# Optimization experiments

Measured on AMD Instinct MI355X. Metric: run time of the kernel, lower is better.

Reference implementation:

```python
import jax, jax.numpy as jnp
import numpy as np

B = 131072          # batch
T = 1024            # num_task_types
D = 1029            # input_dim = 5 + T  (4 scalar feats + contention effect + T one-hot)
H1, H2 = 64, 32     # hidden_dims


def setup_inputs() -> dict:
    key = jax.random.key(0)
    ks = jax.random.split(key, 8)
    x = jax.random.normal(ks[0], (B, D), dtype=jnp.float32)
    contention = jax.random.normal(ks[1], (T, T), dtype=jnp.float32) * 0.1
    # MLP params (Linear uses y = x @ W.T + b in torch; we store W as (in, out))
    w1 = jax.random.normal(ks[2], (D, H1), dtype=jnp.float32) * (1.0 / np.sqrt(D))
    b1 = jnp.zeros((H1,), dtype=jnp.float32)
    w2 = jax.random.normal(ks[3], (H1, H2), dtype=jnp.float32) * (1.0 / np.sqrt(H1))
    b2 = jnp.zeros((H2,), dtype=jnp.float32)
    w3 = jax.random.normal(ks[4], (H2, 1), dtype=jnp.float32) * (1.0 / np.sqrt(H2))
    b3 = jnp.zeros((1,), dtype=jnp.float32)
    return {"x": x, "contention": contention,
            "w1": w1, "b1": b1, "w2": w2, "b2": b2, "w3": w3, "b3": b3}


def reference(x, contention, w1, b1, w2, b2, w3, b3):
    feats = x[:, :4]                          # density, recent_latency, diversity, time_since_same
    density = x[:, 0:1]                       # (B, 1)
    task_onehot = x[:, 4:4 + T]               # (B, T)
    task_id = jnp.argmax(task_onehot, axis=1) # (B,) int
    # vectorized replacement of the per-sample python loop:
    # gather row, mean over columns, scale by density
    contention_effect = jnp.mean(contention[task_id], axis=1, keepdims=True) * density  # (B, 1)
    combined = jnp.concatenate([feats, contention_effect, task_onehot], axis=1)  # (B, 5+T) == (B, D)
    # MLP (dropout is identity in eval mode)
    h = jax.nn.relu(combined @ w1 + b1)
    h = jax.nn.relu(h @ w2 + b2)
    latency = jax.nn.relu(h @ w3 + b3)        # (B, 1)
    return latency[:, 0]                      # squeeze -> (B,)
```

## Files before the change

kernel.cpp:

```cpp
#include <hip/hip_runtime.h>

typedef __bf16 bf16x8 __attribute__((ext_vector_type(8)));
typedef float f32x4 __attribute__((ext_vector_type(4)));

#define ROW_F 1029
#define TMB 64
#define NKB 33

__global__ __launch_bounds__(256) void k_rowmean(const float* __restrict__ cont,
                                                 float* __restrict__ rowmean) {
    __shared__ float red[4];
    int row = blockIdx.x;
    const float4* cr = (const float4*)(cont + (size_t)row * 1024);
    float4 v = cr[threadIdx.x];
    float p = v.x + v.y + v.z + v.w;
    for (int m = 1; m < 64; m <<= 1) p += __shfl_xor(p, m, 64);
    int lane = threadIdx.x & 63, wid = threadIdx.x >> 6;
    if (lane == 0) red[wid] = p;
    __syncthreads();
    if (threadIdx.x == 0)
        rowmean[row] = (red[0] + red[1] + red[2] + red[3]) * (1.0f / 1024.0f);
}

__global__ __launch_bounds__(256) void k_wpack(const float* __restrict__ w1,
                                               __bf16* __restrict__ wfrag) {
    int o = blockIdx.x * 256 + threadIdx.x;
    int j    = o & 7;
    int lane = (o >> 3) & 63;
    int nt   = (o >> 9) & 3;
    int kb   = o >> 11;
    int k = kb * 32 + ((lane >> 4) << 3) + j;
    int n = nt * 16 + (lane & 15);
    float val = 0.0f;
    if (k < 4)          val = w1[k * 64 + n];
    else if (k < 1028)  val = w1[(k + 1) * 64 + n];
    wfrag[o] = (__bf16)val;
}

__global__ __launch_bounds__(256, 4) void k_main(const float* __restrict__ x,
                                                 const float* __restrict__ w1,
                                                 const float* __restrict__ b1,
                                                 const float* __restrict__ w2,
                                                 const float* __restrict__ b2,
                                                 const float* __restrict__ w3,
                                                 const float* __restrict__ b3,
                                                 const float* __restrict__ rowmean,
                                                 const __bf16* __restrict__ wfrag,
                                                 float* __restrict__ out) {
    __shared__ float h1_lds[TMB * 65];

    const int tid = threadIdx.x;
    const int l   = tid & 63;
    const int w   = tid >> 6;
    const int m0  = l & 15;
    const int c   = l >> 4;

    const int row = blockIdx.x * TMB + w * 16 + m0;
    const float* xr = x + (size_t)row * ROW_F + c * 8;
    const f32x4* wfp = (const f32x4*)wfrag;

    f32x4 acc0 = {0.f,0.f,0.f,0.f}, acc1 = {0.f,0.f,0.f,0.f};
    f32x4 acc2 = {0.f,0.f,0.f,0.f}, acc3 = {0.f,0.f,0.f,0.f};
    float best = -1e30f; int bidx = 4; float dens = 0.f;

    {
        float v[8];
        #pragma unroll
        for (int j = 0; j < 8; ++j) v[j] = xr[j];
        if (c == 0) dens = v[0];
        bf16x8 af;
        #pragma unroll
        for (int j = 0; j < 8; ++j) {
            af[j] = (__bf16)v[j];
            int k = c * 8 + j;
            bool ok = (k >= 4) && (v[j] > best);
            best = ok ? v[j] : best;
            bidx = ok ? k : bidx;
        }
        acc0 = __builtin_amdgcn_mfma_f32_16x16x32_bf16(af, __builtin_bit_cast(bf16x8, wfp[0*64 + l]), acc0, 0,0,0);
        acc1 = __builtin_amdgcn_mfma_f32_16x16x32_bf16(af, __builtin_bit_cast(bf16x8, wfp[1*64 + l]), acc1, 0,0,0);
        acc2 = __builtin_amdgcn_mfma_f32_16x16x32_bf16(af, __builtin_bit_cast(bf16x8, wfp[2*64 + l]), acc2, 0,0,0);
        acc3 = __builtin_amdgcn_mfma_f32_16x16x32_bf16(af, __builtin_bit_cast(bf16x8, wfp[3*64 + l]), acc3, 0,0,0);
    }

    for (int kb = 1; kb < 32; ++kb) {
        const float* p = xr + kb * 32;
        float v[8];
        #pragma unroll
        for (int j = 0; j < 8; ++j) v[j] = p[j];
        bf16x8 af;
        int kbase = kb * 32 + c * 8;
        #pragma unroll
        for (int j = 0; j < 8; ++j) {
            af[j] = (__bf16)v[j];
            bool gt = v[j] > best;
            best = gt ? v[j] : best;
            bidx = gt ? (kbase + j) : bidx;
        }
        acc0 = __builtin_amdgcn_mfma_f32_16x16x32_bf16(af, __builtin_bit_cast(bf16x8, wfp[(kb*4+0)*64 + l]), acc0, 0,0,0);
        acc1 = __builtin_amdgcn_mfma_f32_16x16x32_bf16(af, __builtin_bit_cast(bf16x8, wfp[(kb*4+1)*64 + l]), acc1, 0,0,0);
        acc2 = __builtin_amdgcn_mfma_f32_16x16x32_bf16(af, __builtin_bit_cast(bf16x8, wfp[(kb*4+2)*64 + l]), acc2, 0,0,0);
        acc3 = __builtin_amdgcn_mfma_f32_16x16x32_bf16(af, __builtin_bit_cast(bf16x8, wfp[(kb*4+3)*64 + l]), acc3, 0,0,0);
    }

    {
        bf16x8 af;
        #pragma unroll
        for (int j = 0; j < 8; ++j) af[j] = (__bf16)0.f;
        if (c == 0) {
            const float* p = xr + 32 * 32;
            #pragma unroll
            for (int j = 0; j < 4; ++j) {
                float v = p[j];
                af[j] = (__bf16)v;
                bool gt = v > best;
                best = gt ? v : best;
                bidx = gt ? (1024 + j) : bidx;
            }
        }
        acc0 = __builtin_amdgcn_mfma_f32_16x16x32_bf16(af, __builtin_bit_cast(bf16x8, wfp[(32*4+0)*64 + l]), acc0, 0,0,0);
        acc1 = __builtin_amdgcn_mfma_f32_16x16x32_bf16(af, __builtin_bit_cast(bf16x8, wfp[(32*4+1)*64 + l]), acc1, 0,0,0);
        acc2 = __builtin_amdgcn_mfma_f32_16x16x32_bf16(af, __builtin_bit_cast(bf16x8, wfp[(32*4+2)*64 + l]), acc2, 0,0,0);
        acc3 = __builtin_amdgcn_mfma_f32_16x16x32_bf16(af, __builtin_bit_cast(bf16x8, wfp[(32*4+3)*64 + l]), acc3, 0,0,0);
    }

    #pragma unroll
    for (int off = 16; off < 64; off <<= 1) {
        float ob = __shfl_xor(best, off, 64);
        int   oi = __shfl_xor(bidx, off, 64);
        if (ob > best || (ob == best && oi < bidx)) { best = ob; bidx = oi; }
    }
    float ce = 0.f;
    if (c == 0) ce = rowmean[bidx - 4] * dens;

    float ce_r[4];
    #pragma unroll
    for (int r = 0; r < 4; ++r) ce_r[r] = __shfl(ce, c * 4 + r, 64);

    {
        const f32x4* accs[4] = {&acc0, &acc1, &acc2, &acc3};
        #pragma unroll
        for (int nt = 0; nt < 4; ++nt) {
            int n = nt * 16 + m0;
            float w14 = w1[4 * 64 + n];
            float bb  = b1[n];
            #pragma unroll
            for (int r = 0; r < 4; ++r) {
                int m = c * 4 + r;
                float hv = (*accs[nt])[r] + ce_r[r] * w14 + bb;
                h1_lds[(w * 16 + m) * 65 + n] = fmaxf(hv, 0.0f);
            }
        }
    }
    __syncthreads();

    {
        int s  = tid & 15;
        int n2 = s * 2;
        #pragma unroll
        for (int it = 0; it < 4; ++it) {
            int r2 = it * 16 + (tid >> 4);
            float a0 = b2[n2], a1 = b2[n2 + 1];
            const float* hrow = &h1_lds[r2 * 65];
            #pragma unroll 8
            for (int k = 0; k < 64; ++k) {
                float hv = hrow[k];
                float2 wv = *(const float2*)(w2 + k * 32 + n2);
                a0 = fmaf(hv, wv.x, a0);
                a1 = fmaf(hv, wv.y, a1);
            }
            a0 = fmaxf(a0, 0.f); a1 = fmaxf(a1, 0.f);
            float p = a0 * w3[n2] + a1 * w3[n2 + 1];
            p += __shfl_xor(p, 1, 64);
            p += __shfl_xor(p, 2, 64);
            p += __shfl_xor(p, 4, 64);
            p += __shfl_xor(p, 8, 64);
            if (s == 0) out[blockIdx.x * TMB + r2] = fmaxf(p + b3[0], 0.f);
        }
    }
}

extern "C" void kernel_launch(void* const* d_in, const int* in_sizes, int n_in,
                              void* d_out, int out_size, void* d_ws, size_t ws_size,
                              hipStream_t stream) {
    const float* x    = (const float*)d_in[0];
    const float* cont = (const float*)d_in[1];
    const float* w1   = (const float*)d_in[2];
    const float* b1   = (const float*)d_in[3];
    const float* w2   = (const float*)d_in[4];
    const float* b2   = (const float*)d_in[5];
    const float* w3   = (const float*)d_in[6];
    const float* b3   = (const float*)d_in[7];

    __bf16* wfrag   = (__bf16*)d_ws;
    float*  rowmean = (float*)((char*)d_ws + 135168);

    int B = in_sizes[0] / ROW_F;
    float* out = (float*)d_out;

    hipLaunchKernelGGL(k_rowmean, dim3(1024),    dim3(256), 0, stream, cont, rowmean);
    hipLaunchKernelGGL(k_wpack,   dim3(264),     dim3(256), 0, stream, w1, wfrag);
    hipLaunchKernelGGL(k_main,    dim3(B / TMB), dim3(256), 0, stream,
                       x, w1, b1, w2, b2, w3, b3, rowmean, wfrag, out);
}
```

Before: 782.0 us.

## Coalesce x loads via per-wave LDS slab with register prefetch

Each wave now loads its 16 rows of x in coalesced 32-float row segments, using nontemporal loads with a one-block register prefetch. It then transposes them through a per-wave LDS slab into the MFMA A-fragment layout. This replaces the earlier scattered 8-float per-lane strided reads. The layer-2 stage uses per-wave LDS with no block-wide barrier, and launch_bounds drops the occupancy hint. The cost is extra LDS traffic and possibly more register pressure.

After: 792.2 us. About the same (+1.3%).

```diff
diff --git a/kernel.cpp b/kernel.cpp
--- a/kernel.cpp
+++ b/kernel.cpp
@@ -4,8 +4,7 @@
 typedef float f32x4 __attribute__((ext_vector_type(4)));
 
 #define ROW_F 1029
-#define TMB 64
-#define NKB 33
+#define SLAB_STRIDE 36
 
 __global__ __launch_bounds__(256) void k_rowmean(const float* __restrict__ cont,
                                                  float* __restrict__ rowmean) {
@@ -37,91 +36,105 @@
     wfrag[o] = (__bf16)val;
 }
 
-__global__ __launch_bounds__(256, 4) void k_main(const float* __restrict__ x,
-                                                 const float* __restrict__ w1,
-                                                 const float* __restrict__ b1,
-                                                 const float* __restrict__ w2,
-                                                 const float* __restrict__ b2,
-                                                 const float* __restrict__ w3,
-                                                 const float* __restrict__ b3,
-                                                 const float* __restrict__ rowmean,
-                                                 const __bf16* __restrict__ wfrag,
-                                                 float* __restrict__ out) {
-    __shared__ float h1_lds[TMB * 65];
-
-    const int tid = threadIdx.x;
-    const int l   = tid & 63;
-    const int w   = tid >> 6;
-    const int m0  = l & 15;
-    const int c   = l >> 4;
-
-    const int row = blockIdx.x * TMB + w * 16 + m0;
-    const float* xr = x + (size_t)row * ROW_F + c * 8;
+__global__ __launch_bounds__(256) void k_main(const float* __restrict__ x,
+                                              const float* __restrict__ w1,
+                                              const float* __restrict__ b1,
+                                              const float* __restrict__ w2,
+                                              const float* __restrict__ b2,
+                                              const float* __restrict__ w3,
+                                              const float* __restrict__ b3,
+                                              const float* __restrict__ rowmean,
+                                              const __bf16* __restrict__ wfrag,
+                                              float* __restrict__ out) {
+    __shared__ __align__(16) float slab_s[4][16 * SLAB_STRIDE];
+    __shared__ float h1_s[4][16 * 65];
+
+    const int tid  = threadIdx.x;
+    const int l    = tid & 63;
+    const int w    = tid >> 6;
+    const int m0   = l & 15;
+    const int c    = l >> 4;
+    const int c32  = l & 31;
+    const int hsel = l >> 5;
+
+    float* slabw = slab_s[w];
+    float* h1w   = h1_s[w];
+
+    const int rowbase = blockIdx.x * 64 + w * 16;
+    const float* xw = x + (size_t)rowbase * ROW_F;
     const f32x4* wfp = (const f32x4*)wfrag;
 
     f32x4 acc0 = {0.f,0.f,0.f,0.f}, acc1 = {0.f,0.f,0.f,0.f};
     f32x4 acc2 = {0.f,0.f,0.f,0.f}, acc3 = {0.f,0.f,0.f,0.f};
     float best = -1e30f; int bidx = 4; float dens = 0.f;
 
-    {
-        float v[8];
-        #pragma unroll
-        for (int j = 0; j < 8; ++j) v[j] = xr[j];
-        if (c == 0) dens = v[0];
+    float vx[8];
+    #pragma unroll
+    for (int i = 0; i < 8; ++i)
+        vx[i] = __builtin_nontemporal_load(xw + (size_t)(2*i + hsel) * ROW_F + c32);
+
+    for (int kb = 0; kb < 33; ++kb) {
+        float vn[8];
+        if (kb < 31) {
+            #pragma unroll
+            for (int i = 0; i < 8; ++i)
+                vn[i] = __builtin_nontemporal_load(xw + (size_t)(2*i + hsel) * ROW_F + (kb + 1) * 32 + c32);
+        } else if (kb == 31) {
+            #pragma unroll
+            for (int i = 0; i < 8; ++i)
+                vn[i] = (c32 < 5)
+                    ? __builtin_nontemporal_load(xw + (size_t)(2*i + hsel) * ROW_F + 1024 + c32)
+                    : 0.0f;
+        }
+
+        #pragma unroll
+        for (int i = 0; i < 8; ++i)
+            slabw[(2*i + hsel) * SLAB_STRIDE + c32] = vx[i];
+
+        const f32x4* afp = (const f32x4*)(slabw + m0 * SLAB_STRIDE + c * 8);
+        f32x4 a0 = afp[0], a1 = afp[1];
+        float vj[8];
+        #pragma unroll
+        for (int jj = 0; jj < 4; ++jj) { vj[jj] = a0[jj]; vj[4 + jj] = a1[jj]; }
         bf16x8 af;
         #pragma unroll
-        for (int j = 0; j < 8; ++j) {
-            af[j] = (__bf16)v[j];
-            int k = c * 8 + j;
-            bool ok = (k >= 4) && (v[j] > best);
-            best = ok ? v[j] : best;
-            bidx = ok ? k : bidx;
-        }
-        acc0 = __builtin_amdgcn_mfma_f32_16x16x32_bf16(af, __builtin_bit_cast(bf16x8, wfp[0*64 + l]), acc0, 0,0,0);
-        acc1 = __builtin_amdgcn_mfma_f32_16x16x32_bf16(af, __builtin_bit_cast(bf16x8, wfp[1*64 + l]), acc1, 0,0,0);
-        acc2 = __builtin_amdgcn_mfma_f32_16x16x32_bf16(af, __builtin_bit_cast(bf16x8, wfp[2*64 + l]), acc2, 0,0,0);
-        acc3 = __builtin_amdgcn_mfma_f32_16x16x32_bf16(af, __builtin_bit_cast(bf16x8, wfp[3*64 + l]), acc3, 0,0,0);
-    }
-
-    for (int kb = 1; kb < 32; ++kb) {
-        const float* p = xr + kb * 32;
-        float v[8];
-        #pragma unroll
-        for (int j = 0; j < 8; ++j) v[j] = p[j];
-        bf16x8 af;
-        int kbase = kb * 32 + c * 8;
-        #pragma unroll
-        for (int j = 0; j < 8; ++j) {
-            af[j] = (__bf16)v[j];
-            bool gt = v[j] > best;
-            best = gt ? v[j] : best;
-            bidx = gt ? (kbase + j) : bidx;
-        }
-        acc0 = __builtin_amdgcn_mfma_f32_16x16x32_bf16(af, __builtin_bit_cast(bf16x8, wfp[(kb*4+0)*64 + l]), acc0, 0,0,0);
-        acc1 = __builtin_amdgcn_mfma_f32_16x16x32_bf16(af, __builtin_bit_cast(bf16x8, wfp[(kb*4+1)*64 + l]), acc1, 0,0,0);
-        acc2 = __builtin_amdgcn_mfma_f32_16x16x32_bf16(af, __builtin_bit_cast(bf16x8, wfp[(kb*4+2)*64 + l]), acc2, 0,0,0);
-        acc3 = __builtin_amdgcn_mfma_f32_16x16x32_bf16(af, __builtin_bit_cast(bf16x8, wfp[(kb*4+3)*64 + l]), acc3, 0,0,0);
-    }
-
-    {
-        bf16x8 af;
-        #pragma unroll
-        for (int j = 0; j < 8; ++j) af[j] = (__bf16)0.f;
-        if (c == 0) {
-            const float* p = xr + 32 * 32;
-            #pragma unroll
-            for (int j = 0; j < 4; ++j) {
-                float v = p[j];
-                af[j] = (__bf16)v;
-                bool gt = v > best;
-                best = gt ? v : best;
-                bidx = gt ? (1024 + j) : bidx;
-            }
-        }
-        acc0 = __builtin_amdgcn_mfma_f32_16x16x32_bf16(af, __builtin_bit_cast(bf16x8, wfp[(32*4+0)*64 + l]), acc0, 0,0,0);
-        acc1 = __builtin_amdgcn_mfma_f32_16x16x32_bf16(af, __builtin_bit_cast(bf16x8, wfp[(32*4+1)*64 + l]), acc1, 0,0,0);
-        acc2 = __builtin_amdgcn_mfma_f32_16x16x32_bf16(af, __builtin_bit_cast(bf16x8, wfp[(32*4+2)*64 + l]), acc2, 0,0,0);
-        acc3 = __builtin_amdgcn_mfma_f32_16x16x32_bf16(af, __builtin_bit_cast(bf16x8, wfp[(32*4+3)*64 + l]), acc3, 0,0,0);
+        for (int j = 0; j < 8; ++j) af[j] = (__bf16)vj[j];
+
+        if (kb == 0) {
+            if (c == 0) dens = vj[0];
+            #pragma unroll
+            for (int j = 0; j < 8; ++j) {
+                int k = c * 8 + j;
+                bool ok = (k >= 4) && (vj[j] > best);
+                best = ok ? vj[j] : best;
+                bidx = ok ? k : bidx;
+            }
+        } else if (kb == 32) {
+            if (c == 0) {
+                #pragma unroll
+                for (int j = 0; j < 4; ++j) {
+                    bool gt = vj[j] > best;
+                    best = gt ? vj[j] : best;
+                    bidx = gt ? (1024 + j) : bidx;
+                }
+            }
+        } else {
+            int kbase = kb * 32 + c * 8;
+            #pragma unroll
+            for (int j = 0; j < 8; ++j) {
+                bool gt = vj[j] > best;
+                best = gt ? vj[j] : best;
+                bidx = gt ? (kbase + j) : bidx;
+            }
+        }
+
+        acc0 = __builtin_amdgcn_mfma_f32_16x16x32_bf16(af, __builtin_bit_cast(bf16x8, wfp[(kb*4 + 0)*64 + l]), acc0, 0,0,0);
+        acc1 = __builtin_amdgcn_mfma_f32_16x16x32_bf16(af, __builtin_bit_cast(bf16x8, wfp[(kb*4 + 1)*64 + l]), acc1, 0,0,0);
+        acc2 = __builtin_amdgcn_mfma_f32_16x16x32_bf16(af, __builtin_bit_cast(bf16x8, wfp[(kb*4 + 2)*64 + l]), acc2, 0,0,0);
+        acc3 = __builtin_amdgcn_mfma_f32_16x16x32_bf16(af, __builtin_bit_cast(bf16x8, wfp[(kb*4 + 3)*64 + l]), acc3, 0,0,0);
+
+        #pragma unroll
+        for (int i = 0; i < 8; ++i) vx[i] = vn[i];
     }
 
     #pragma unroll
@@ -132,7 +145,6 @@
     }
     float ce = 0.f;
     if (c == 0) ce = rowmean[bidx - 4] * dens;
-
     float ce_r[4];
     #pragma unroll
     for (int r = 0; r < 4; ++r) ce_r[r] = __shfl(ce, c * 4 + r, 64);
@@ -148,20 +160,19 @@
             for (int r = 0; r < 4; ++r) {
                 int m = c * 4 + r;
                 float hv = (*accs[nt])[r] + ce_r[r] * w14 + bb;
-                h1_lds[(w * 16 + m) * 65 + n] = fmaxf(hv, 0.0f);
-            }
-        }
-    }
-    __syncthreads();
+                h1w[m * 65 + n] = fmaxf(hv, 0.0f);
+            }
+        }
+    }
 
     {
-        int s  = tid & 15;
+        int s  = l & 15;
         int n2 = s * 2;
         #pragma unroll
         for (int it = 0; it < 4; ++it) {
-            int r2 = it * 16 + (tid >> 4);
+            int r2 = it * 4 + c;
             float a0 = b2[n2], a1 = b2[n2 + 1];
-            const float* hrow = &h1_lds[r2 * 65];
+            const float* hrow = &h1w[r2 * 65];
             #pragma unroll 8
             for (int k = 0; k < 64; ++k) {
                 float hv = hrow[k];
@@ -175,7 +186,7 @@
             p += __shfl_xor(p, 2, 64);
             p += __shfl_xor(p, 4, 64);
             p += __shfl_xor(p, 8, 64);
-            if (s == 0) out[blockIdx.x * TMB + r2] = fmaxf(p + b3[0], 0.f);
+            if (s == 0) out[rowbase + r2] = fmaxf(p + b3[0], 0.f);
         }
     }
 }
@@ -198,8 +209,8 @@
     int B = in_sizes[0] / ROW_F;
     float* out = (float*)d_out;
 
-    hipLaunchKernelGGL(k_rowmean, dim3(1024),    dim3(256), 0, stream, cont, rowmean);
-    hipLaunchKernelGGL(k_wpack,   dim3(264),     dim3(256), 0, stream, w1, wfrag);
-    hipLaunchKernelGGL(k_main,    dim3(B / TMB), dim3(256), 0, stream,
+    hipLaunchKernelGGL(k_rowmean, dim3(1024),   dim3(256), 0, stream, cont, rowmean);
+    hipLaunchKernelGGL(k_wpack,   dim3(264),    dim3(256), 0, stream, w1, wfrag);
+    hipLaunchKernelGGL(k_main,    dim3(B / 64), dim3(256), 0, stream,
                        x, w1, b1, w2, b2, w3, b3, rowmean, wfrag, out);
 }
```
